# Kernel optimization log

Hardware: AMD Instinct MI355X
Metric: run time of the kernel (lower is better)

## Reference

```python
import jax, jax.numpy as jnp
import numpy as np

T = 5       # Newton-Schulz iterations
EPS = 1e-5


def setup_inputs() -> dict:
    key = jax.random.key(0)
    k1, k2 = jax.random.split(key)
    N, F = 500000, 128
    X = jax.random.normal(k1, (N, F), dtype=jnp.float32)
    # running_rot buffer: random orthogonal rotation (eye at init; use QR for a non-trivial one)
    M = jax.random.normal(k2, (1, F, F), dtype=jnp.float32)
    Q, _ = jnp.linalg.qr(M)
    return {"X": X, "running_rot": Q.astype(jnp.float32)}


def _whiten(X):
    # iterative_normalization_py.forward, training path, g=1 group
    x = X.T[None]                              # [g=1, d, m]
    d, m = x.shape[1], x.shape[2]
    mean = jnp.mean(x, axis=-1, keepdims=True)
    xc = x - mean                              # centered [1, d, m]
    I = jnp.eye(d, dtype=X.dtype)[None]
    # Sigma = eps*I + xc xc^T / m  (baddbmm with beta=eps, alpha=1/m)
    Sigma = EPS * I + jnp.einsum('gdm,gem->gde', xc, xc) / m
    rTr = 1.0 / jnp.trace(Sigma, axis1=1, axis2=2)[:, None, None]  # 1/tr(Sigma)
    Sn = Sigma * rTr                           # trace-normalized covariance
    P = I
    for _ in range(T):                         # P_{k+1} = 1.5 P_k - 0.5 P_k^3 Sn
        P = 1.5 * P - 0.5 * (P @ P @ P @ Sn)
    wm = P * jnp.sqrt(rTr)                     # whitening matrix = Sigma^{-1/2} (approx)
    xn = wm @ xc                               # [1, d, m]
    return xn[0].T                             # back to [N, F]


def reference(X, running_rot):
    Xn = _whiten(X)                            # [N, F]
    # X_hat = einsum('bgc,gdc->bgd', X_hat, running_rot) with g=1
    out = jnp.einsum('nc,dc->nd', Xn, running_rot[0])
    return out
```

## Files before the change

### kernel.cpp

```cpp
#include <hip/hip_runtime.h>
#include <math.h>

#define NROWS  500000
#define NCHK   7813
#define EPSV   1e-5f

typedef __bf16 bf16_t;
typedef __bf16 bf16x4 __attribute__((ext_vector_type(4)));
typedef __bf16 bf16x8 __attribute__((ext_vector_type(8)));
typedef float  f32x4  __attribute__((ext_vector_type(4)));

static const size_t GT_OFF   = 131072;
static const size_t WB_OFF   = 327680;
static const size_t MEAN_OFF = 360448;
static const size_t BIAS_OFF = 360960;
static const size_t CS_OFF   = 393216;
static const size_t GRAM_OFF = 1048576;

__global__ __launch_bounds__(256) void k_stats(const float* __restrict__ X,
        float* __restrict__ csPart, float* __restrict__ gramPart) {
    __shared__ bf16_t sxtT[2][8192];
    __shared__ float  scs[256][4];
    const int t    = threadIdx.x;
    const int lane = t & 63;
    const int w    = t >> 6;
    const int oct  = t >> 5;
    const int fg4  = t & 31;
    const int cl   = lane & 15;
    const int kq   = lane >> 4;
    const int G    = gridDim.x;

    f32x4 acc[2][8];
    #pragma unroll
    for (int a = 0; a < 2; a++)
        #pragma unroll
        for (int b = 0; b < 8; b++)
            acc[a][b] = (f32x4){0.f, 0.f, 0.f, 0.f};
    float cs0 = 0.f, cs1 = 0.f, cs2 = 0.f, cs3 = 0.f;

    f32x4 R[8];

    auto KF = [](int f) { return (f ^ (f >> 3)) & 7; };

    auto GLOADC = [&](int ch) {
        const size_t row0 = (size_t)ch << 6;
        #pragma unroll
        for (int i = 0; i < 8; i++) {
            const size_t row = row0 + oct * 8 + i;
            R[i] = (row < NROWS)
                 ? *reinterpret_cast<const f32x4*>(X + row * 128 + fg4 * 4)
                 : (f32x4){0.f, 0.f, 0.f, 0.f};
        }
    };
    auto DSWRITEC = [&](int buf) {
        #pragma unroll
        for (int i = 0; i < 8; i++) {
            cs0 += R[i][0]; cs1 += R[i][1]; cs2 += R[i][2]; cs3 += R[i][3];
        }
        bf16_t* S = sxtT[buf];
        #pragma unroll
        for (int j = 0; j < 4; j++) {
            const int f = fg4 * 4 + j;
            const int g = oct ^ KF(f);
            bf16x8 v;
            #pragma unroll
            for (int i = 0; i < 8; i++) v[i] = (bf16_t)R[i][j];
            *reinterpret_cast<bf16x8*>(&S[f * 64 + g * 8]) = v;
        }
    };
    auto MFMAC = [&](int buf) {
        const bf16_t* S = sxtT[buf];
        #pragma unroll
        for (int kb = 0; kb < 2; kb++) {
            const int gq = kb * 4 + kq;
            bf16x8 fa[2];
            #pragma unroll
            for (int a = 0; a < 2; a++) {
                const int f = (w * 2 + a) * 16 + cl;
                fa[a] = *reinterpret_cast<const bf16x8*>(&S[f * 64 + ((gq ^ KF(f)) << 3)]);
            }
            #pragma unroll
            for (int b = 0; b < 8; b++) {
                const int f = b * 16 + cl;
                const bf16x8 fb = *reinterpret_cast<const bf16x8*>(&S[f * 64 + ((gq ^ KF(f)) << 3)]);
                acc[0][b] = __builtin_amdgcn_mfma_f32_16x16x32_bf16(fa[0], fb, acc[0][b], 0, 0, 0);
                acc[1][b] = __builtin_amdgcn_mfma_f32_16x16x32_bf16(fa[1], fb, acc[1][b], 0, 0, 0);
            }
        }
    };

    int ch0 = blockIdx.x;
    GLOADC(ch0);
    DSWRITEC(0);
    __syncthreads();
    for (;;) {
        const int ch1 = ch0 + G;
        const bool v1 = ch1 < NCHK;
        if (v1) GLOADC(ch1);
        MFMAC(0);
        if (v1) DSWRITEC(1);
        __syncthreads();
        if (!v1) break;
        const int ch2 = ch1 + G;
        const bool v2 = ch2 < NCHK;
        if (v2) GLOADC(ch2);
        MFMAC(1);
        if (v2) DSWRITEC(0);
        __syncthreads();
        if (!v2) break;
        ch0 = ch2;
    }

    float* gp = gramPart + (size_t)blockIdx.x * 16384;
    #pragma unroll
    for (int a = 0; a < 2; a++)
        #pragma unroll
        for (int b = 0; b < 8; b++)
            #pragma unroll
            for (int r = 0; r < 4; r++) {
                const int row = (w * 2 + a) * 16 + kq * 4 + r;
                const int col = b * 16 + cl;
                gp[row * 128 + col] = acc[a][b][r];
            }
    scs[t][0] = cs0; scs[t][1] = cs1; scs[t][2] = cs2; scs[t][3] = cs3;
    __syncthreads();
    if (t < 128) {
        float s = 0.f;
        #pragma unroll
        for (int q = 0; q < 8; q++) s += scs[q * 32 + (t >> 2)][t & 3];
        csPart[(size_t)blockIdx.x * 128 + t] = s;
    }
}

__global__ __launch_bounds__(256) void k_gred(const float* __restrict__ gramPart,
        const float* __restrict__ csPart, float* __restrict__ gramTot,
        float* __restrict__ mean, int G) {
    const int t = threadIdx.x;
    const int b = blockIdx.x;
    if (b == 256) {
        if (t < 128) {
            float s = 0.f;
            int g = 0;
            for (; g + 8 <= G; g += 8) {
                float p[8];
                #pragma unroll
                for (int u = 0; u < 8; u++) p[u] = csPart[(size_t)(g + u) * 128 + t];
                s += ((p[0] + p[1]) + (p[2] + p[3])) + ((p[4] + p[5]) + (p[6] + p[7]));
            }
            for (; g < G; g++) s += csPart[(size_t)g * 128 + t];
            mean[t] = s * (1.0f / (float)NROWS);
        }
        return;
    }
    const int e  = b * 64 + (t & 63);
    const int sl = t >> 6;
    float s = 0.f;
    int g = sl;
    for (; g + 28 < G; g += 32) {
        float v[8];
        #pragma unroll
        for (int u = 0; u < 8; u++)
            v[u] = gramPart[(size_t)(g + 4 * u) * 16384 + e];
        s += ((v[0] + v[1]) + (v[2] + v[3])) + ((v[4] + v[5]) + (v[6] + v[7]));
    }
    for (; g < G; g += 4)
        s += gramPart[(size_t)g * 16384 + e];
    __shared__ float red[4][64];
    red[sl][t & 63] = s;
    __syncthreads();
    if (t < 64)
        gramTot[b * 64 + t] = (red[0][t] + red[1][t]) + (red[2][t] + red[3][t]);
}

__global__ __launch_bounds__(512) void k_ns(const float* __restrict__ gramTot,
        const float* __restrict__ mean, const float* __restrict__ Rg,
        bf16_t* __restrict__ Wb, float* __restrict__ bias) {
    __shared__ bf16_t sPh[16384], sPl[16384], sSn[16384], sTT[16384];
    const int t = threadIdx.x;
    const int w = t >> 6, lane = t & 63;
    const int cl = lane & 15, kq = lane >> 4;

    float sig[32];
    float tr = 0.f;
    #pragma unroll
    for (int i = 0; i < 32; i++) {
        const int e = t + (i << 9);
        const int r = e >> 7, c = e & 127;
        float s = gramTot[e] * (1.0f / (float)NROWS) - mean[r] * mean[c];
        if (r == c) { s += EPSV; tr += s; }
        sig[i] = s;
    }
    float* rs = reinterpret_cast<float*>(sTT);
    rs[t] = tr;
    __syncthreads();
    #pragma unroll
    for (int off = 256; off > 0; off >>= 1) {
        if (t < off) rs[t] += rs[t + off];
        __syncthreads();
    }
    const float rTr = 1.0f / rs[0];
    __syncthreads();
    #pragma unroll
    for (int i = 0; i < 32; i++) {
        const int e = t + (i << 9);
        const int r = e >> 7, c = e & 127;
        const int ix = r * 128 + (c ^ ((r & 7) << 3));
        const float snv = sig[i] * rTr;
        sSn[ix] = (bf16_t)snv;
        const float p0 = ((r == c) ? 1.5f : 0.f) - 0.5f * snv;
        const bf16_t ph = (bf16_t)p0;
        sPh[ix] = ph;
        sPl[ix] = (bf16_t)(p0 - (float)ph);
    }
    __syncthreads();

    f32x4 acc[8];
    auto NSMM = [&](const bf16_t* __restrict__ Bm) {
        #pragma unroll
        for (int ct = 0; ct < 8; ct++) acc[ct] = (f32x4){0.f, 0.f, 0.f, 0.f};
        const int ra = w * 16 + cl;
        #pragma unroll
        for (int kb = 0; kb < 4; kb++) {
            const int k0 = kb * 32 + kq * 8;
            const int ia = ra * 128 + (k0 ^ ((ra & 7) << 3));
            const bf16x8 ah = *reinterpret_cast<const bf16x8*>(&sPh[ia]);
            const bf16x8 al = *reinterpret_cast<const bf16x8*>(&sPl[ia]);
            #pragma unroll
            for (int ct = 0; ct < 8; ct++) {
                const int rb = ct * 16 + cl;
                const bf16x8 bb = *reinterpret_cast<const bf16x8*>(
                    &Bm[rb * 128 + (k0 ^ ((rb & 7) << 3))]);
                acc[ct] = __builtin_amdgcn_mfma_f32_16x16x32_bf16(ah, bb, acc[ct], 0, 0, 0);
                acc[ct] = __builtin_amdgcn_mfma_f32_16x16x32_bf16(al, bb, acc[ct], 0, 0, 0);
            }
        }
    };
    auto WRT = [&](bf16_t* __restrict__ D) {
        #pragma unroll
        for (int ct = 0; ct < 8; ct++)
            #pragma unroll
            for (int r = 0; r < 4; r++) {
                const int ro = w * 16 + kq * 4 + r, co = ct * 16 + cl;
                D[ro * 128 + (co ^ ((ro & 7) << 3))] = (bf16_t)acc[ct][r];
            }
    };

    for (int it = 0; it < 4; it++) {
        NSMM(sSn);
        WRT(sTT);
        __syncthreads();
        NSMM(sTT);
        __syncthreads();
        WRT(sTT);
        __syncthreads();
        NSMM(sTT);
        #pragma unroll
        for (int ct = 0; ct < 8; ct++)
            #pragma unroll
            for (int r = 0; r < 4; r++) {
                const int ro = w * 16 + kq * 4 + r, co = ct * 16 + cl;
                const int ix = ro * 128 + (co ^ ((ro & 7) << 3));
                const float pold = (float)sPh[ix] + (float)sPl[ix];
                const float pn = 1.5f * pold - 0.5f * acc[ct][r];
                const bf16_t ph = (bf16_t)pn;
                sPh[ix] = ph;
                sPl[ix] = (bf16_t)(pn - (float)ph);
            }
        __syncthreads();
    }

    const float scal = sqrtf(rTr);
    #pragma unroll
    for (int ct = 0; ct < 8; ct++) acc[ct] = (f32x4){0.f, 0.f, 0.f, 0.f};
    const int ra = w * 16 + cl;
    #pragma unroll
    for (int kb = 0; kb < 4; kb++) {
        const int k0 = kb * 32 + kq * 8;
        const float4 rv0 = *reinterpret_cast<const float4*>(&Rg[ra * 128 + k0]);
        const float4 rv1 = *reinterpret_cast<const float4*>(&Rg[ra * 128 + k0 + 4]);
        const float rv[8] = {rv0.x, rv0.y, rv0.z, rv0.w, rv1.x, rv1.y, rv1.z, rv1.w};
        bf16x8 ah, al;
        #pragma unroll
        for (int j = 0; j < 8; j++) {
            ah[j] = (bf16_t)rv[j];
            al[j] = (bf16_t)(rv[j] - (float)ah[j]);
        }
        #pragma unroll
        for (int ct = 0; ct < 8; ct++) {
            const int rb = ct * 16 + cl;
            const int ib = rb * 128 + (k0 ^ ((rb & 7) << 3));
            const bf16x8 bh = *reinterpret_cast<const bf16x8*>(&sPh[ib]);
            const bf16x8 bl = *reinterpret_cast<const bf16x8*>(&sPl[ib]);
            acc[ct] = __builtin_amdgcn_mfma_f32_16x16x32_bf16(ah, bh, acc[ct], 0, 0, 0);
            acc[ct] = __builtin_amdgcn_mfma_f32_16x16x32_bf16(al, bh, acc[ct], 0, 0, 0);
            acc[ct] = __builtin_amdgcn_mfma_f32_16x16x32_bf16(ah, bl, acc[ct], 0, 0, 0);
        }
    }
    float pb[4] = {0.f, 0.f, 0.f, 0.f};
    #pragma unroll
    for (int ct = 0; ct < 8; ct++) {
        const float mv = mean[ct * 16 + cl];
        #pragma unroll
        for (int r = 0; r < 4; r++) {
            const float wv = acc[ct][r] * scal;
            Wb[(w * 16 + kq * 4 + r) * 128 + ct * 16 + cl] = (bf16_t)wv;
            pb[r] += wv * mv;
        }
    }
    #pragma unroll
    for (int r = 0; r < 4; r++) {
        float v = pb[r];
        v += __shfl_xor(v, 1);
        v += __shfl_xor(v, 2);
        v += __shfl_xor(v, 4);
        v += __shfl_xor(v, 8);
        if (cl == 0) bias[w * 16 + kq * 4 + r] = v;
    }
}

__global__ __launch_bounds__(256) void k_out(const float* __restrict__ X,
        const bf16_t* __restrict__ Wb, const float* __restrict__ bias,
        float* __restrict__ out) {
    __shared__ bf16_t sW[128][136];
    __shared__ float sBias[128];
    const int t = threadIdx.x;
    const int w = t >> 6, lane = t & 63;
    const int cl = lane & 15, kq = lane >> 4;
    const size_t rowbase = (size_t)blockIdx.x * 64 + (size_t)w * 16;
    const bool valid = rowbase < NROWS;

    float4 B[8];
    {
        const float* xr = X + (rowbase + cl) * 128;
        #pragma unroll
        for (int kb = 0; kb < 4; kb++) {
            B[2*kb]   = valid ? *reinterpret_cast<const float4*>(xr + kb*32 + kq*8)
                              : float4{0.f,0.f,0.f,0.f};
            B[2*kb+1] = valid ? *reinterpret_cast<const float4*>(xr + kb*32 + kq*8 + 4)
                              : float4{0.f,0.f,0.f,0.f};
        }
    }
    #pragma unroll
    for (int i = 0; i < 16; i++) {
        const int idx = (t + (i << 8)) << 2;
        *reinterpret_cast<bf16x4*>(&sW[idx >> 7][idx & 127]) =
            *reinterpret_cast<const bf16x4*>(&Wb[idx]);
    }
    if (t < 128) sBias[t] = bias[t];
    __syncthreads();
    if (!valid) return;

    bf16x8 ah[4], al[4];
    #pragma unroll
    for (int kb = 0; kb < 4; kb++) {
        const float4 v0 = B[2*kb], v1 = B[2*kb+1];
        const float xv[8] = {v0.x, v0.y, v0.z, v0.w, v1.x, v1.y, v1.z, v1.w};
        bf16x8 h, l;
        #pragma unroll
        for (int j = 0; j < 8; j++) {
            h[j] = (bf16_t)xv[j];
            l[j] = (bf16_t)(xv[j] - (float)h[j]);
        }
        ah[kb] = h; al[kb] = l;
    }
    #pragma unroll
    for (int ct = 0; ct < 8; ct++) {
        f32x4 acc = (f32x4){0.f, 0.f, 0.f, 0.f};
        const int d = ct * 16 + cl;
        #pragma unroll
        for (int kb = 0; kb < 4; kb++) {
            const bf16x8 bf = *reinterpret_cast<const bf16x8*>(&sW[d][kb*32 + kq*8]);
            acc = __builtin_amdgcn_mfma_f32_16x16x32_bf16(al[kb], bf, acc, 0, 0, 0);
            acc = __builtin_amdgcn_mfma_f32_16x16x32_bf16(ah[kb], bf, acc, 0, 0, 0);
        }
        const float bc = sBias[d];
        #pragma unroll
        for (int r = 0; r < 4; r++)
            out[(rowbase + kq*4 + r) * 128 + d] = acc[r] - bc;
    }
}

extern "C" void kernel_launch(void* const* d_in, const int* in_sizes, int n_in,
                              void* d_out, int out_size, void* d_ws, size_t ws_size,
                              hipStream_t stream) {
    const float* X = (const float*)d_in[0];
    const float* R = (const float*)d_in[1];
    float* out = (float*)d_out;
    char* ws = (char*)d_ws;
    float*  gramTot = (float*)(ws + GT_OFF);
    bf16_t* Wb      = (bf16_t*)(ws + WB_OFF);
    float*  mean    = (float*)(ws + MEAN_OFF);
    float*  bias    = (float*)(ws + BIAS_OFF);
    float*  csPart  = (float*)(ws + CS_OFF);

    int G = 512;
    size_t avail = (ws_size > GRAM_OFF) ? (ws_size - GRAM_OFF) : 0;
    if (avail < (size_t)G * 65536) {
        G = (int)(avail / 65536);
        if (G < 1) G = 1;
        if (G > 512) G = 512;
    }
    float* gramPart = (float*)(ws + GRAM_OFF);

    k_stats<<<dim3(G), dim3(256), 0, stream>>>(X, csPart, gramPart);
    k_gred<<<dim3(257), dim3(256), 0, stream>>>(gramPart, csPart, gramTot, mean, G);
    k_ns<<<dim3(1), dim3(512), 0, stream>>>(gramTot, mean, R, Wb, bias);
    k_out<<<dim3(NCHK), dim3(256), 0, stream>>>(X, Wb, bias, out);
}
```

Baseline: 222.7 us.

## Restructure Newton-Schulz kernel to 4 waves with 32-row tiles and transposed stores

The single-block Newton-Schulz kernel drops from 512 to 256 threads, and each wave now computes two 16-row MFMA tiles. This reuses each B-fragment load across twice as many MFMAs. Intermediate products are stored transposed as packed bf16x4 vectors instead of scalar bf16, and the trace is computed from the diagonal alone before Sigma is built. The output kernel also walks tiles in reverse order, likely to hit L2-resident rows of X left by the stats pass. The trade-off is fewer waves on the serial single-block stage.

```diff
diff --git a/kernel.cpp b/kernel.cpp
--- a/kernel.cpp
+++ b/kernel.cpp
@@ -172,7 +172,7 @@
         gramTot[b * 64 + t] = (red[0][t] + red[1][t]) + (red[2][t] + red[3][t]);
 }
 
-__global__ __launch_bounds__(512) void k_ns(const float* __restrict__ gramTot,
+__global__ __launch_bounds__(256) void k_ns(const float* __restrict__ gramTot,
         const float* __restrict__ mean, const float* __restrict__ Rg,
         bf16_t* __restrict__ Wb, float* __restrict__ bias) {
     __shared__ bf16_t sPh[16384], sPl[16384], sSn[16384], sTT[16384];
@@ -180,32 +180,28 @@
     const int w = t >> 6, lane = t & 63;
     const int cl = lane & 15, kq = lane >> 4;
 
-    float sig[32];
-    float tr = 0.f;
-    #pragma unroll
-    for (int i = 0; i < 32; i++) {
-        const int e = t + (i << 9);
+    float* rs = reinterpret_cast<float*>(sTT);
+    float dv = 0.f;
+    if (t < 128) {
+        const float m = mean[t];
+        dv = gramTot[t * 129] * (1.0f / (float)NROWS) - m * m + EPSV;
+    }
+    rs[t] = dv;
+    __syncthreads();
+    #pragma unroll
+    for (int off = 128; off > 0; off >>= 1) {
+        if (t < off) rs[t] += rs[t + off];
+        __syncthreads();
+    }
+    const float rTr = 1.0f / rs[0];
+    __syncthreads();
+    for (int i = 0; i < 64; i++) {
+        const int e = t + (i << 8);
         const int r = e >> 7, c = e & 127;
         float s = gramTot[e] * (1.0f / (float)NROWS) - mean[r] * mean[c];
-        if (r == c) { s += EPSV; tr += s; }
-        sig[i] = s;
-    }
-    float* rs = reinterpret_cast<float*>(sTT);
-    rs[t] = tr;
-    __syncthreads();
-    #pragma unroll
-    for (int off = 256; off > 0; off >>= 1) {
-        if (t < off) rs[t] += rs[t + off];
-        __syncthreads();
-    }
-    const float rTr = 1.0f / rs[0];
-    __syncthreads();
-    #pragma unroll
-    for (int i = 0; i < 32; i++) {
-        const int e = t + (i << 9);
-        const int r = e >> 7, c = e & 127;
+        if (r == c) s += EPSV;
         const int ix = r * 128 + (c ^ ((r & 7) << 3));
-        const float snv = sig[i] * rTr;
+        const float snv = s * rTr;
         sSn[ix] = (bf16_t)snv;
         const float p0 = ((r == c) ? 1.5f : 0.f) - 0.5f * snv;
         const bf16_t ph = (bf16_t)p0;
@@ -214,35 +210,47 @@
     }
     __syncthreads();
 
-    f32x4 acc[8];
+    f32x4 acc[2][8];
     auto NSMM = [&](const bf16_t* __restrict__ Bm) {
         #pragma unroll
-        for (int ct = 0; ct < 8; ct++) acc[ct] = (f32x4){0.f, 0.f, 0.f, 0.f};
-        const int ra = w * 16 + cl;
+        for (int a = 0; a < 2; a++)
+            #pragma unroll
+            for (int ct = 0; ct < 8; ct++) acc[a][ct] = (f32x4){0.f, 0.f, 0.f, 0.f};
         #pragma unroll
         for (int kb = 0; kb < 4; kb++) {
             const int k0 = kb * 32 + kq * 8;
-            const int ia = ra * 128 + (k0 ^ ((ra & 7) << 3));
-            const bf16x8 ah = *reinterpret_cast<const bf16x8*>(&sPh[ia]);
-            const bf16x8 al = *reinterpret_cast<const bf16x8*>(&sPl[ia]);
+            bf16x8 ah[2], al[2];
+            #pragma unroll
+            for (int a = 0; a < 2; a++) {
+                const int ra = w * 32 + a * 16 + cl;
+                const int ia = ra * 128 + (k0 ^ ((ra & 7) << 3));
+                ah[a] = *reinterpret_cast<const bf16x8*>(&sPh[ia]);
+                al[a] = *reinterpret_cast<const bf16x8*>(&sPl[ia]);
+            }
             #pragma unroll
             for (int ct = 0; ct < 8; ct++) {
                 const int rb = ct * 16 + cl;
                 const bf16x8 bb = *reinterpret_cast<const bf16x8*>(
                     &Bm[rb * 128 + (k0 ^ ((rb & 7) << 3))]);
-                acc[ct] = __builtin_amdgcn_mfma_f32_16x16x32_bf16(ah, bb, acc[ct], 0, 0, 0);
-                acc[ct] = __builtin_amdgcn_mfma_f32_16x16x32_bf16(al, bb, acc[ct], 0, 0, 0);
+                acc[0][ct] = __builtin_amdgcn_mfma_f32_16x16x32_bf16(ah[0], bb, acc[0][ct], 0, 0, 0);
+                acc[0][ct] = __builtin_amdgcn_mfma_f32_16x16x32_bf16(al[0], bb, acc[0][ct], 0, 0, 0);
+                acc[1][ct] = __builtin_amdgcn_mfma_f32_16x16x32_bf16(ah[1], bb, acc[1][ct], 0, 0, 0);
+                acc[1][ct] = __builtin_amdgcn_mfma_f32_16x16x32_bf16(al[1], bb, acc[1][ct], 0, 0, 0);
             }
         }
     };
     auto WRT = [&](bf16_t* __restrict__ D) {
         #pragma unroll
-        for (int ct = 0; ct < 8; ct++)
-            #pragma unroll
-            for (int r = 0; r < 4; r++) {
-                const int ro = w * 16 + kq * 4 + r, co = ct * 16 + cl;
-                D[ro * 128 + (co ^ ((ro & 7) << 3))] = (bf16_t)acc[ct][r];
-            }
+        for (int a = 0; a < 2; a++) {
+            const int ro0 = w * 32 + a * 16 + kq * 4;
+            #pragma unroll
+            for (int ct = 0; ct < 8; ct++) {
+                const int co = ct * 16 + cl;
+                bf16x4 v = { (bf16_t)acc[a][ct][0], (bf16_t)acc[a][ct][1],
+                             (bf16_t)acc[a][ct][2], (bf16_t)acc[a][ct][3] };
+                *reinterpret_cast<bf16x4*>(&D[co * 128 + (ro0 ^ ((co & 7) << 3))]) = v;
+            }
+        }
     };
 
     for (int it = 0; it < 4; it++) {
@@ -255,35 +263,51 @@
         __syncthreads();
         NSMM(sTT);
         #pragma unroll
-        for (int ct = 0; ct < 8; ct++)
-            #pragma unroll
-            for (int r = 0; r < 4; r++) {
-                const int ro = w * 16 + kq * 4 + r, co = ct * 16 + cl;
-                const int ix = ro * 128 + (co ^ ((ro & 7) << 3));
-                const float pold = (float)sPh[ix] + (float)sPl[ix];
-                const float pn = 1.5f * pold - 0.5f * acc[ct][r];
-                const bf16_t ph = (bf16_t)pn;
-                sPh[ix] = ph;
-                sPl[ix] = (bf16_t)(pn - (float)ph);
-            }
+        for (int a = 0; a < 2; a++) {
+            const int ro0 = w * 32 + a * 16 + kq * 4;
+            #pragma unroll
+            for (int ct = 0; ct < 8; ct++) {
+                const int co = ct * 16 + cl;
+                const int ix = co * 128 + (ro0 ^ ((co & 7) << 3));
+                bf16x4 ph4 = *reinterpret_cast<const bf16x4*>(&sPh[ix]);
+                bf16x4 pl4 = *reinterpret_cast<const bf16x4*>(&sPl[ix]);
+                bf16x4 nh, nl;
+                #pragma unroll
+                for (int r = 0; r < 4; r++) {
+                    const float pold = (float)ph4[r] + (float)pl4[r];
+                    const float pn = 1.5f * pold - 0.5f * acc[a][ct][r];
+                    nh[r] = (bf16_t)pn;
+                    nl[r] = (bf16_t)(pn - (float)nh[r]);
+                }
+                *reinterpret_cast<bf16x4*>(&sPh[ix]) = nh;
+                *reinterpret_cast<bf16x4*>(&sPl[ix]) = nl;
+            }
+        }
         __syncthreads();
     }
 
     const float scal = sqrtf(rTr);
     #pragma unroll
-    for (int ct = 0; ct < 8; ct++) acc[ct] = (f32x4){0.f, 0.f, 0.f, 0.f};
-    const int ra = w * 16 + cl;
+    for (int a = 0; a < 2; a++)
+        #pragma unroll
+        for (int ct = 0; ct < 8; ct++) acc[a][ct] = (f32x4){0.f, 0.f, 0.f, 0.f};
     #pragma unroll
     for (int kb = 0; kb < 4; kb++) {
         const int k0 = kb * 32 + kq * 8;
-        const float4 rv0 = *reinterpret_cast<const float4*>(&Rg[ra * 128 + k0]);
-        const float4 rv1 = *reinterpret_cast<const float4*>(&Rg[ra * 128 + k0 + 4]);
-        const float rv[8] = {rv0.x, rv0.y, rv0.z, rv0.w, rv1.x, rv1.y, rv1.z, rv1.w};
-        bf16x8 ah, al;
-        #pragma unroll
-        for (int j = 0; j < 8; j++) {
-            ah[j] = (bf16_t)rv[j];
-            al[j] = (bf16_t)(rv[j] - (float)ah[j]);
+        bf16x8 ah[2], al[2];
+        #pragma unroll
+        for (int a = 0; a < 2; a++) {
+            const int ra = w * 32 + a * 16 + cl;
+            const float4 rv0 = *reinterpret_cast<const float4*>(&Rg[ra * 128 + k0]);
+            const float4 rv1 = *reinterpret_cast<const float4*>(&Rg[ra * 128 + k0 + 4]);
+            const float rv[8] = {rv0.x, rv0.y, rv0.z, rv0.w, rv1.x, rv1.y, rv1.z, rv1.w};
+            bf16x8 h, l;
+            #pragma unroll
+            for (int j = 0; j < 8; j++) {
+                h[j] = (bf16_t)rv[j];
+                l[j] = (bf16_t)(rv[j] - (float)h[j]);
+            }
+            ah[a] = h; al[a] = l;
         }
         #pragma unroll
         for (int ct = 0; ct < 8; ct++) {
@@ -291,30 +315,36 @@
             const int ib = rb * 128 + (k0 ^ ((rb & 7) << 3));
             const bf16x8 bh = *reinterpret_cast<const bf16x8*>(&sPh[ib]);
             const bf16x8 bl = *reinterpret_cast<const bf16x8*>(&sPl[ib]);
-            acc[ct] = __builtin_amdgcn_mfma_f32_16x16x32_bf16(ah, bh, acc[ct], 0, 0, 0);
-            acc[ct] = __builtin_amdgcn_mfma_f32_16x16x32_bf16(al, bh, acc[ct], 0, 0, 0);
-            acc[ct] = __builtin_amdgcn_mfma_f32_16x16x32_bf16(ah, bl, acc[ct], 0, 0, 0);
-        }
-    }
-    float pb[4] = {0.f, 0.f, 0.f, 0.f};
-    #pragma unroll
-    for (int ct = 0; ct < 8; ct++) {
-        const float mv = mean[ct * 16 + cl];
+            #pragma unroll
+            for (int a = 0; a < 2; a++) {
+                acc[a][ct] = __builtin_amdgcn_mfma_f32_16x16x32_bf16(ah[a], bh, acc[a][ct], 0, 0, 0);
+                acc[a][ct] = __builtin_amdgcn_mfma_f32_16x16x32_bf16(al[a], bh, acc[a][ct], 0, 0, 0);
+                acc[a][ct] = __builtin_amdgcn_mfma_f32_16x16x32_bf16(ah[a], bl, acc[a][ct], 0, 0, 0);
+            }
+        }
+    }
+    #pragma unroll
+    for (int a = 0; a < 2; a++) {
+        float pb[4] = {0.f, 0.f, 0.f, 0.f};
+        #pragma unroll
+        for (int ct = 0; ct < 8; ct++) {
+            const float mv = mean[ct * 16 + cl];
+            #pragma unroll
+            for (int r = 0; r < 4; r++) {
+                const float wv = acc[a][ct][r] * scal;
+                Wb[(w * 32 + a * 16 + kq * 4 + r) * 128 + ct * 16 + cl] = (bf16_t)wv;
+                pb[r] += wv * mv;
+            }
+        }
         #pragma unroll
         for (int r = 0; r < 4; r++) {
-            const float wv = acc[ct][r] * scal;
-            Wb[(w * 16 + kq * 4 + r) * 128 + ct * 16 + cl] = (bf16_t)wv;
-            pb[r] += wv * mv;
-        }
-    }
-    #pragma unroll
-    for (int r = 0; r < 4; r++) {
-        float v = pb[r];
-        v += __shfl_xor(v, 1);
-        v += __shfl_xor(v, 2);
-        v += __shfl_xor(v, 4);
-        v += __shfl_xor(v, 8);
-        if (cl == 0) bias[w * 16 + kq * 4 + r] = v;
+            float v = pb[r];
+            v += __shfl_xor(v, 1);
+            v += __shfl_xor(v, 2);
+            v += __shfl_xor(v, 4);
+            v += __shfl_xor(v, 8);
+            if (cl == 0) bias[w * 32 + a * 16 + kq * 4 + r] = v;
+        }
     }
 }
 
@@ -326,7 +356,8 @@
     const int t = threadIdx.x;
     const int w = t >> 6, lane = t & 63;
     const int cl = lane & 15, kq = lane >> 4;
-    const size_t rowbase = (size_t)blockIdx.x * 64 + (size_t)w * 16;
+    const int tile = NCHK - 1 - blockIdx.x;
+    const size_t rowbase = (size_t)tile * 64 + (size_t)w * 16;
     const bool valid = rowbase < NROWS;
 
     float4 B[8];
@@ -404,6 +435,6 @@
 
     k_stats<<<dim3(G), dim3(256), 0, stream>>>(X, csPart, gramPart);
     k_gred<<<dim3(257), dim3(256), 0, stream>>>(gramPart, csPart, gramTot, mean, G);
-    k_ns<<<dim3(1), dim3(512), 0, stream>>>(gramTot, mean, R, Wb, bias);
+    k_ns<<<dim3(1), dim3(256), 0, stream>>>(gramTot, mean, R, Wb, bias);
     k_out<<<dim3(NCHK), dim3(256), 0, stream>>>(X, Wb, bias, out);
 }
```

Measured after the change: 219.5 us. About the same (-1.5%).
